# Kernel tuning notes

Measured on AMD Instinct MI355X. Metric: run time of the kernel, lower is better.

## Reference

```python
import jax, jax.numpy as jnp
import numpy as np

T, B, P, Q, WW, WF, C = 7, 512, 200, 64, 64, 256, 10
N = B * P
SIGMA = 0.1


def _lin(key, fin, fout):
    kw, kb = jax.random.split(key)
    s = 1.0 / np.sqrt(fin)
    return (jax.random.uniform(kw, (fin, fout), minval=-s, maxval=s),
            jax.random.uniform(kb, (fout,), minval=-s, maxval=s))


def setup_inputs() -> dict:
    key = jax.random.key(0)
    ks = jax.random.split(key, 9)
    diagms = jax.random.normal(ks[0], (T, N, 2), dtype=jnp.float32)
    # repeat_interleave(arange(B), counts): equal-sized segments of P points
    seg_ids = jnp.tile(jnp.repeat(jnp.arange(B, dtype=jnp.int32), P), (T, 1))
    theta = jax.random.normal(ks[1], (Q, 2), dtype=jnp.float32)
    w1, b1 = _lin(ks[2], 2, WW)
    w2, b2 = _lin(ks[3], WW, WW)
    w3, b3 = _lin(ks[4], WW, 1)
    r1, rb1 = _lin(ks[5], T * Q, WF)
    r2, rb2 = _lin(ks[6], WF, WF)
    r3, rb3 = _lin(ks[7], WF, C)
    return dict(diagms=diagms, seg_ids=seg_ids, theta=theta,
                w1=w1, b1=b1, w2=w2, b2=b2, w3=w3, b3=b3,
                r1=r1, rb1=rb1, r2=r2, rb2=rb2, r3=r3, rb3=rb3)


def reference(diagms, seg_ids, theta, w1, b1, w2, b2, w3, b3,
              r1, rb1, r2, rb2, r3, rb3):
    # gaussian kernel: exp(-||x - theta||^2 / (2 sigma^2)), cdist expanded
    diff = diagms[:, :, None, :] - theta[None, None, :, :]      # [T,N,Q,2]
    rep = jnp.exp(-jnp.sum(diff * diff, axis=-1) / (2.0 * SIGMA ** 2))  # [T,N,Q]
    # weight MLP on raw (birth,death) coords, shared across types
    h = jax.nn.relu(diagms @ w1 + b1)
    h = jax.nn.relu(h @ w2 + b2)
    w = jax.nn.sigmoid(h @ w3 + b3)                              # [T,N,1]
    rep = w * rep
    # global_mean_pool per diagram type via segment sum
    def pool(r, s):
        sums = jax.ops.segment_sum(r, s, num_segments=B)         # [B,Q]
        cnts = jax.ops.segment_sum(jnp.ones((r.shape[0],), r.dtype), s,
                                   num_segments=B)
        return sums / jnp.maximum(cnts, 1.0)[:, None]
    pooled = jax.vmap(pool)(rep, seg_ids)                        # [T,B,Q]
    topo = jnp.transpose(pooled, (1, 0, 2)).reshape(B, T * Q)    # cat over types
    # final MLP rho
    z = jax.nn.relu(topo @ r1 + rb1)
    z = jax.nn.relu(z @ r2 + rb2)
    return z @ r3 + rb3                                          # [B,C]
```

## Files before the change

### kernel.cpp

```cpp
#include <hip/hip_runtime.h>
#include <hip/hip_bf16.h>
#include <math.h>

#define TT 7
#define BB 512
#define PP 200
#define QQ 64
#define WWH 64
#define WF 256
#define CC 10
#define NN (BB * PP)
#define TQ (TT * QQ)

typedef __attribute__((ext_vector_type(8))) short short8;
typedef __attribute__((ext_vector_type(4))) float f32x4;

static __device__ __forceinline__ unsigned short f2bf(float f) {
    __hip_bfloat16 b = __float2bfloat16(f);
    return *reinterpret_cast<unsigned short*>(&b);
}

__global__ __launch_bounds__(256, 4) void point_weight_kernel(
    const float* __restrict__ diagms,
    const float* __restrict__ w1,
    const float* __restrict__ b1,
    const float* __restrict__ w2,
    const float* __restrict__ b2,
    const float* __restrict__ w3,
    const float* __restrict__ b3,
    float* __restrict__ w_out)
{
    __shared__ unsigned short Hl[256 * 64];
    __shared__ unsigned short W2T[64 * 64];

    const int tid  = threadIdx.x;
    const int lane = tid & 63;
    const int wv   = tid >> 6;

    {
        const int n  = tid & 63;
        const int j0 = (tid >> 6) * 16;
#pragma unroll
        for (int jj = 0; jj < 16; ++jj) {
            const int j = j0 + jj;
            const float v = w2[j * WWH + n];
            const int off = n * 64 + ((((j >> 3) ^ (n & 7))) << 3) + (j & 7);
            W2T[off] = f2bf(v);
        }
    }

    {
        const int p = tid;
        const float2 d = reinterpret_cast<const float2*>(diagms)[(size_t)blockIdx.x * 256 + p];
        const float x = d.x, y = d.y;
        uint4* Hrow = reinterpret_cast<uint4*>(Hl);
#pragma unroll
        for (int i = 0; i < 8; ++i) {
            unsigned int pk[4];
#pragma unroll
            for (int e = 0; e < 4; ++e) {
                const int j = i * 8 + 2 * e;
                const float h0 = fmaxf(fmaf(x, w1[j],     fmaf(y, w1[WWH + j],     b1[j])),     0.0f);
                const float h1 = fmaxf(fmaf(x, w1[j + 1], fmaf(y, w1[WWH + j + 1], b1[j + 1])), 0.0f);
                pk[e] = (unsigned int)f2bf(h0) | ((unsigned int)f2bf(h1) << 16);
            }
            uint4 v; v.x = pk[0]; v.y = pk[1]; v.z = pk[2]; v.w = pk[3];
            Hrow[p * 8 + (i ^ (p & 7))] = v;
        }
    }

    __syncthreads();

    float b2v[4], w3v[4];
#pragma unroll
    for (int nt = 0; nt < 4; ++nt) {
        b2v[nt] = b2[nt * 16 + (lane & 15)];
        w3v[nt] = w3[nt * 16 + (lane & 15)];
    }
    const float b3s = b3[0];

    short8 bf[2][4];
#pragma unroll
    for (int s = 0; s < 2; ++s) {
#pragma unroll
        for (int nt = 0; nt < 4; ++nt) {
            const int n = nt * 16 + (lane & 15);
            const int slot = ((lane >> 4) + s * 4) ^ (lane & 7);
            bf[s][nt] = reinterpret_cast<const short8*>(W2T)[n * 8 + slot];
        }
    }

    const int wave_p0 = wv * 64;
    const size_t out_base = (size_t)blockIdx.x * 256;

#pragma unroll 1
    for (int m = 0; m < 4; ++m) {
        f32x4 acc[4];
#pragma unroll
        for (int nt = 0; nt < 4; ++nt) acc[nt] = (f32x4){0.f, 0.f, 0.f, 0.f};

#pragma unroll
        for (int s = 0; s < 2; ++s) {
            const int p = wave_p0 + m * 16 + (lane & 15);
            const int slot = ((lane >> 4) + s * 4) ^ (lane & 7);
            const short8 af = reinterpret_cast<const short8*>(Hl)[p * 8 + slot];
#pragma unroll
            for (int nt = 0; nt < 4; ++nt) {
                acc[nt] = __builtin_amdgcn_mfma_f32_16x16x32_bf16(af, bf[s][nt], acc[nt], 0, 0, 0);
            }
        }

        float sum0 = 0.f, sum1 = 0.f, sum2 = 0.f, sum3 = 0.f;
#pragma unroll
        for (int nt = 0; nt < 4; ++nt) {
            sum0 = fmaf(fmaxf(acc[nt][0] + b2v[nt], 0.f), w3v[nt], sum0);
            sum1 = fmaf(fmaxf(acc[nt][1] + b2v[nt], 0.f), w3v[nt], sum1);
            sum2 = fmaf(fmaxf(acc[nt][2] + b2v[nt], 0.f), w3v[nt], sum2);
            sum3 = fmaf(fmaxf(acc[nt][3] + b2v[nt], 0.f), w3v[nt], sum3);
        }
#pragma unroll
        for (int off = 1; off < 16; off <<= 1) {
            sum0 += __shfl_xor(sum0, off, 64);
            sum1 += __shfl_xor(sum1, off, 64);
            sum2 += __shfl_xor(sum2, off, 64);
            sum3 += __shfl_xor(sum3, off, 64);
        }
        const int r_sel = lane & 15;
        if (r_sel < 4) {
            const float sv = (r_sel == 0) ? sum0 : (r_sel == 1) ? sum1
                           : (r_sel == 2) ? sum2 : sum3;
            const float wa = sv + b3s;
            const float wsig = 1.0f / (1.0f + __expf(-wa));
            const int prow = wave_p0 + m * 16 + ((lane >> 4) << 2) + r_sel;
            w_out[out_base + prow] = wsig;
        }
    }
}

#define NEG50_OVER_LN2 (-72.13475204444817f)

__global__ __launch_bounds__(256) void rep_pool_kernel(
    const float* __restrict__ diagms,
    const float* __restrict__ theta,
    const float* __restrict__ w_in,
    float* __restrict__ pooled)
{
    const int bid = blockIdx.x;
    const int t = bid >> 9;
    const int b = bid & (BB - 1);
    const int tid = threadIdx.x;

    __shared__ float px[PP];
    __shared__ float py[PP];
    __shared__ float wv[PP];

    if (tid < PP) {
        const int n = t * NN + b * PP + tid;
        const float2 d = reinterpret_cast<const float2*>(diagms)[n];
        px[tid] = d.x;
        py[tid] = d.y;
        wv[tid] = w_in[n];
    }
    __syncthreads();

    const int q = tid & (QQ - 1);
    const int g = tid >> 6;
    const float2 th = reinterpret_cast<const float2*>(theta)[q];
    const float tx = th.x;
    const float ty = th.y;

    float acc = 0.0f;
    const int p0 = g * (PP / 4);
#pragma unroll 5
    for (int p = p0; p < p0 + PP / 4; ++p) {
        const float dx = px[p] - tx;
        const float dy = py[p] - ty;
        acc = fmaf(wv[p], exp2f(fmaf(dx, dx, dy * dy) * NEG50_OVER_LN2), acc);
    }

    __shared__ float part[4][QQ];
    part[g][q] = acc;
    __syncthreads();

    if (tid < QQ) {
        const float s = (part[0][tid] + part[1][tid]) + (part[2][tid] + part[3][tid]);
        pooled[b * TQ + t * QQ + tid] = s * (1.0f / (float)PP);
    }
}

#define K3_ROWS 2
__global__ __launch_bounds__(512) void rho_kernel(
    const float* __restrict__ pooled,
    const float* __restrict__ r1,
    const float* __restrict__ rb1,
    const float* __restrict__ r2,
    const float* __restrict__ rb2,
    const float* __restrict__ r3,
    const float* __restrict__ rb3,
    float* __restrict__ out)
{
    const int b0 = blockIdx.x * K3_ROWS;
    const int tid = threadIdx.x;
    const int k = tid & (WF - 1);
    const int g = tid >> 8;

    __shared__ float z1[K3_ROWS][WF];
    __shared__ float z2[K3_ROWS][WF];
    __shared__ float part[2][K3_ROWS][WF];

    const float* __restrict__ tp0 = pooled + (size_t)b0 * TQ;
    const float* __restrict__ tp1 = tp0 + TQ;

    float a0 = 0.0f, a1 = 0.0f;
    {
        const int i0 = g * (TQ / 2);
#pragma unroll 4
        for (int i = i0; i < i0 + TQ / 2; ++i) {
            const float rv = r1[i * WF + k];
            a0 = fmaf(tp0[i], rv, a0);
            a1 = fmaf(tp1[i], rv, a1);
        }
    }
    part[g][0][k] = a0;
    part[g][1][k] = a1;
    __syncthreads();
    if (g == 0) {
        z1[0][k] = fmaxf(part[0][0][k] + part[1][0][k] + rb1[k], 0.0f);
        z1[1][k] = fmaxf(part[0][1][k] + part[1][1][k] + rb1[k], 0.0f);
    }
    __syncthreads();

    float c0 = 0.0f, c1 = 0.0f;
    {
        const int i0 = g * (WF / 2);
#pragma unroll 4
        for (int i = i0; i < i0 + WF / 2; ++i) {
            const float rv = r2[i * WF + k];
            c0 = fmaf(z1[0][i], rv, c0);
            c1 = fmaf(z1[1][i], rv, c1);
        }
    }
    part[g][0][k] = c0;
    part[g][1][k] = c1;
    __syncthreads();
    if (g == 0) {
        z2[0][k] = fmaxf(part[0][0][k] + part[1][0][k] + rb2[k], 0.0f);
        z2[1][k] = fmaxf(part[0][1][k] + part[1][1][k] + rb2[k], 0.0f);
    }
    __syncthreads();

    if (tid < K3_ROWS * CC) {
        const int r = tid / CC;
        const int c = tid % CC;
        float acc = rb3[c];
#pragma unroll 8
        for (int i = 0; i < WF; ++i) acc = fmaf(z2[r][i], r3[i * CC + c], acc);
        out[(size_t)(b0 + r) * CC + c] = acc;
    }
}

extern "C" void kernel_launch(void* const* d_in, const int* in_sizes, int n_in,
                              void* d_out, int out_size, void* d_ws, size_t ws_size,
                              hipStream_t stream)
{
    const float* diagms = (const float*)d_in[0];
    const float* theta  = (const float*)d_in[2];
    const float* w1     = (const float*)d_in[3];
    const float* b1     = (const float*)d_in[4];
    const float* w2     = (const float*)d_in[5];
    const float* b2     = (const float*)d_in[6];
    const float* w3     = (const float*)d_in[7];
    const float* b3     = (const float*)d_in[8];
    const float* r1     = (const float*)d_in[9];
    const float* rb1    = (const float*)d_in[10];
    const float* r2     = (const float*)d_in[11];
    const float* rb2    = (const float*)d_in[12];
    const float* r3     = (const float*)d_in[13];
    const float* rb3    = (const float*)d_in[14];
    float* out = (float*)d_out;

    float* w_buf  = (float*)d_ws;
    float* pooled = w_buf + (size_t)TT * NN;

    const int total = TT * NN;

    point_weight_kernel<<<total / 256, 256, 0, stream>>>(
        diagms, w1, b1, w2, b2, w3, b3, w_buf);

    rep_pool_kernel<<<TT * BB, 256, 0, stream>>>(diagms, theta, w_buf, pooled);

    rho_kernel<<<BB / K3_ROWS, 512, 0, stream>>>(pooled, r1, rb1, r2, rb2, r3, rb3, out);
}
```

Before: 152.4 us.

## Restructure rho MLP kernel with staged inputs, prefetched weights and shuffle reduction

```diff
diff --git a/kernel.cpp b/kernel.cpp
--- a/kernel.cpp
+++ b/kernel.cpp
@@ -189,7 +189,7 @@
 }
 
 #define K3_ROWS 2
-__global__ __launch_bounds__(512) void rho_kernel(
+__global__ __launch_bounds__(256, 2) void rho_kernel(
     const float* __restrict__ pooled,
     const float* __restrict__ r1,
     const float* __restrict__ rb1,
@@ -201,61 +201,116 @@
 {
     const int b0 = blockIdx.x * K3_ROWS;
     const int tid = threadIdx.x;
-    const int k = tid & (WF - 1);
-    const int g = tid >> 8;
-
+
+    __shared__ float tp[K3_ROWS * TQ];
     __shared__ float z1[K3_ROWS][WF];
     __shared__ float z2[K3_ROWS][WF];
-    __shared__ float part[2][K3_ROWS][WF];
-
-    const float* __restrict__ tp0 = pooled + (size_t)b0 * TQ;
-    const float* __restrict__ tp1 = tp0 + TQ;
-
-    float a0 = 0.0f, a1 = 0.0f;
-    {
-        const int i0 = g * (TQ / 2);
-#pragma unroll 4
-        for (int i = i0; i < i0 + TQ / 2; ++i) {
-            const float rv = r1[i * WF + k];
-            a0 = fmaf(tp0[i], rv, a0);
-            a1 = fmaf(tp1[i], rv, a1);
-        }
-    }
-    part[g][0][k] = a0;
-    part[g][1][k] = a1;
-    __syncthreads();
-    if (g == 0) {
-        z1[0][k] = fmaxf(part[0][0][k] + part[1][0][k] + rb1[k], 0.0f);
-        z1[1][k] = fmaxf(part[0][1][k] + part[1][1][k] + rb1[k], 0.0f);
-    }
-    __syncthreads();
-
-    float c0 = 0.0f, c1 = 0.0f;
-    {
-        const int i0 = g * (WF / 2);
-#pragma unroll 4
-        for (int i = i0; i < i0 + WF / 2; ++i) {
-            const float rv = r2[i * WF + k];
-            c0 = fmaf(z1[0][i], rv, c0);
-            c1 = fmaf(z1[1][i], rv, c1);
-        }
-    }
-    part[g][0][k] = c0;
-    part[g][1][k] = c1;
-    __syncthreads();
-    if (g == 0) {
-        z2[0][k] = fmaxf(part[0][0][k] + part[1][0][k] + rb2[k], 0.0f);
-        z2[1][k] = fmaxf(part[0][1][k] + part[1][1][k] + rb2[k], 0.0f);
-    }
-    __syncthreads();
-
-    if (tid < K3_ROWS * CC) {
-        const int r = tid / CC;
-        const int c = tid % CC;
-        float acc = rb3[c];
-#pragma unroll 8
-        for (int i = 0; i < WF; ++i) acc = fmaf(z2[r][i], r3[i * CC + c], acc);
-        out[(size_t)(b0 + r) * CC + c] = acc;
+    __shared__ float red[4][K3_ROWS][CC];
+
+    {
+        const float* src = pooled + (size_t)b0 * TQ;
+#pragma unroll
+        for (int j = 0; j < K3_ROWS * TQ; j += 256) {
+            const int idx = j + tid;
+            if (idx < K3_ROWS * TQ) tp[idx] = src[idx];
+        }
+    }
+    __syncthreads();
+
+    {
+        float acc0 = rb1[tid], acc1 = rb1[tid];
+        const float* r1c = r1 + tid;
+        float rv0[8], rv1[8];
+#pragma unroll
+        for (int e = 0; e < 8; ++e) rv0[e] = r1c[e * WF];
+#pragma unroll 1
+        for (int i0 = 0; i0 < TQ; i0 += 16) {
+#pragma unroll
+            for (int e = 0; e < 8; ++e) rv1[e] = r1c[(i0 + 8 + e) * WF];
+#pragma unroll
+            for (int e = 0; e < 8; ++e) {
+                acc0 = fmaf(tp[i0 + e],      rv0[e], acc0);
+                acc1 = fmaf(tp[TQ + i0 + e], rv0[e], acc1);
+            }
+            if (i0 + 16 < TQ) {
+#pragma unroll
+                for (int e = 0; e < 8; ++e) rv0[e] = r1c[(i0 + 16 + e) * WF];
+            }
+#pragma unroll
+            for (int e = 0; e < 8; ++e) {
+                acc0 = fmaf(tp[i0 + 8 + e],      rv1[e], acc0);
+                acc1 = fmaf(tp[TQ + i0 + 8 + e], rv1[e], acc1);
+            }
+        }
+        z1[0][tid] = fmaxf(acc0, 0.0f);
+        z1[1][tid] = fmaxf(acc1, 0.0f);
+    }
+    __syncthreads();
+
+    {
+        float acc0 = rb2[tid], acc1 = rb2[tid];
+        const float* r2c = r2 + tid;
+        float rv0[8], rv1[8];
+#pragma unroll
+        for (int e = 0; e < 8; ++e) rv0[e] = r2c[e * WF];
+#pragma unroll 1
+        for (int i0 = 0; i0 < WF; i0 += 16) {
+#pragma unroll
+            for (int e = 0; e < 8; ++e) rv1[e] = r2c[(i0 + 8 + e) * WF];
+#pragma unroll
+            for (int e = 0; e < 8; ++e) {
+                acc0 = fmaf(z1[0][i0 + e], rv0[e], acc0);
+                acc1 = fmaf(z1[1][i0 + e], rv0[e], acc1);
+            }
+            if (i0 + 16 < WF) {
+#pragma unroll
+                for (int e = 0; e < 8; ++e) rv0[e] = r2c[(i0 + 16 + e) * WF];
+            }
+#pragma unroll
+            for (int e = 0; e < 8; ++e) {
+                acc0 = fmaf(z1[0][i0 + 8 + e], rv1[e], acc0);
+                acc1 = fmaf(z1[1][i0 + 8 + e], rv1[e], acc1);
+            }
+        }
+        z2[0][tid] = fmaxf(acc0, 0.0f);
+        z2[1][tid] = fmaxf(acc1, 0.0f);
+    }
+    __syncthreads();
+
+    {
+        const int lane = tid & 63;
+        const int wvi  = tid >> 6;
+        const float za = z2[0][tid];
+        const float zb = z2[1][tid];
+        float p0[CC], p1[CC];
+#pragma unroll
+        for (int c = 0; c < CC; ++c) {
+            const float rc = r3[tid * CC + c];
+            p0[c] = za * rc;
+            p1[c] = zb * rc;
+        }
+#pragma unroll
+        for (int off = 32; off >= 1; off >>= 1) {
+#pragma unroll
+            for (int c = 0; c < CC; ++c) {
+                p0[c] += __shfl_xor(p0[c], off, 64);
+                p1[c] += __shfl_xor(p1[c], off, 64);
+            }
+        }
+        if (lane == 0) {
+#pragma unroll
+            for (int c = 0; c < CC; ++c) {
+                red[wvi][0][c] = p0[c];
+                red[wvi][1][c] = p1[c];
+            }
+        }
+        __syncthreads();
+        if (tid < K3_ROWS * CC) {
+            const int r = tid / CC;
+            const int c = tid % CC;
+            out[(size_t)(b0 + r) * CC + c] =
+                red[0][r][c] + red[1][r][c] + red[2][r][c] + red[3][r][c] + rb3[c];
+        }
     }
 }
 
@@ -289,5 +344,5 @@
 
     rep_pool_kernel<<<TT * BB, 256, 0, stream>>>(diagms, theta, w_buf, pooled);
 
-    rho_kernel<<<BB / K3_ROWS, 512, 0, stream>>>(pooled, r1, rb1, r2, rb2, r3, rb3, out);
-}
+    rho_kernel<<<BB / K3_ROWS, 256, 0, stream>>>(pooled, r1, rb1, r2, rb2, r3, rb3, out);
+}
```

After: 145.4 us. 1.05x faster.
